# Kernel tuning notes

Measured on AMD Instinct MI355X. Metric: run time of the kernel, lower is better.

Reference implementation:

```python
import jax, jax.numpy as jnp
import numpy as np
from math import sqrt

DIM = 64
N_HEADS = 12
B, T = 4, 2048


def setup_inputs() -> dict:
    key = jax.random.key(0)
    ks = jax.random.split(key, 5)
    scale = 1.0 / sqrt(DIM)
    x = jax.random.normal(ks[0], (B, T, DIM), dtype=jnp.float32)
    # torch Linear(dim, h*dim) weight is (h*dim, dim); store transposed (dim, h*dim)
    Wq = jax.random.uniform(ks[1], (DIM, N_HEADS * DIM), dtype=jnp.float32, minval=-scale, maxval=scale)
    Wk = jax.random.uniform(ks[2], (DIM, N_HEADS * DIM), dtype=jnp.float32, minval=-scale, maxval=scale)
    Wv = jax.random.uniform(ks[3], (DIM, N_HEADS * DIM), dtype=jnp.float32, minval=-scale, maxval=scale)
    # finalDense: Linear(h*dim, dim) -> stored (h*dim, dim)
    Wo = jax.random.uniform(ks[4], (N_HEADS * DIM, DIM), dtype=jnp.float32,
                            minval=-1.0 / sqrt(N_HEADS * DIM), maxval=1.0 / sqrt(N_HEADS * DIM))
    return {"x": x, "Wq": Wq, "Wk": Wk, "Wv": Wv, "Wo": Wo}


def reference(x, Wq, Wk, Wv, Wo):
    b, t, k = x.shape
    h = Wq.shape[1] // k
    # NOTE: the original module does .view(b,t,h,k).view(b*h,t,k), a flat
    # row-major memory reinterpretation (NOT a head transpose). jnp.reshape
    # is the same flat reshape, so this is faithful.
    Q = (x @ Wq).reshape(b * h, t, k)
    K = (x @ Wk).reshape(b * h, t, k)
    V = (x @ Wv).reshape(b * h, t, k)
    # W[b,i,j] = sum_k K[b,i,k] * Q[b,j,k], scaled; softmax over j (last dim)
    W = jnp.einsum('bik,bjk->bij', K, Q) / sqrt(k)
    W = jax.nn.softmax(W, axis=2)
    Z = jnp.einsum('bij,bjk->bik', W, V)  # (b*h, t, k)
    Z = Z.reshape(b, t, h * k)  # flat reinterpretation, matches torch views
    return Z @ Wo
```

## Files before the change

### kernel.cpp

```cpp
#include <hip/hip_runtime.h>
#include <hip/hip_bf16.h>


#define DIM 64
#define NH 12
#define HD 768
#define BT 8192
#define TSEQ 2048
#define NSLICE 48
#define SLICE (TSEQ*DIM)

#define LDQ 72
#define LDP 72
#define LDT 72

typedef unsigned short ushort;
typedef __attribute__((ext_vector_type(8))) short bf16x8;
typedef __attribute__((ext_vector_type(4))) float f32x4;

#define SCALE2 0.18033688011112042f

__device__ __forceinline__ ushort f2b(float f) {
    union { float f; unsigned int i; } v; v.f = f;
    unsigned int x = v.i;
    return (ushort)((x + 0x7fffu + ((x >> 16) & 1u)) >> 16);
}

__global__ __launch_bounds__(256) void prep_w(
    const float* __restrict__ Wq, const float* __restrict__ Wk,
    const float* __restrict__ Wv, const float* __restrict__ Wo,
    ushort* __restrict__ Wt, ushort* __restrict__ Wot)
{
    __shared__ float tile[64][65];
    int bx = blockIdx.x;
    int z = bx / 12, bt = bx % 12;
    const float* __restrict__ IN = (z == 0) ? Wq : (z == 1) ? Wk : (z == 2) ? Wv : Wo;
    int inStride  = (z < 3) ? HD : DIM;
    int outStride = (z < 3) ? DIM : HD;
    int rbase = (z < 3) ? 0 : bt * 64;
    int cbase = (z < 3) ? bt * 64 : 0;
    ushort* __restrict__ OUT = (z < 3) ? (Wt + (size_t)z * HD * DIM) : Wot;
    int t = threadIdx.x;
    int r = t >> 2, c0 = (t & 3) * 16;
    #pragma unroll
    for (int cc = 0; cc < 16; cc += 4) {
        float4 a = *(const float4*)&IN[(size_t)(rbase + r) * inStride + cbase + c0 + cc];
        tile[r][c0 + cc] = a.x; tile[r][c0 + cc + 1] = a.y;
        tile[r][c0 + cc + 2] = a.z; tile[r][c0 + cc + 3] = a.w;
    }
    __syncthreads();
    int cl = t >> 2, r0 = (t & 3) * 16;
    ushort tmp[16] __attribute__((aligned(16)));
    #pragma unroll
    for (int rr = 0; rr < 16; ++rr) tmp[rr] = f2b(tile[r0 + rr][cl]);
    *(float4*)&OUT[(size_t)(cbase + cl) * outStride + rbase + r0] = *(const float4*)tmp;
    *(float4*)&OUT[(size_t)(cbase + cl) * outStride + rbase + r0 + 8] = *(const float4*)&tmp[8];
}

__global__ __launch_bounds__(256) void qkv_kernel(
    const float* __restrict__ x, const ushort* __restrict__ Wt,
    ushort* __restrict__ Q, ushort* __restrict__ K, ushort* __restrict__ V)
{
    int rt = blockIdx.x, yg = blockIdx.y;
    int t = threadIdx.x, w = t >> 6, lane = t & 63;
    int ln = lane & 15, q = lane >> 4;
    int m0 = rt * 64 + w * 16;

    float4 xa = *(const float4*)&x[(size_t)(m0 + ln) * DIM + q * 8];
    float4 xb_ = *(const float4*)&x[(size_t)(m0 + ln) * DIM + q * 8 + 4];
    float4 xc = *(const float4*)&x[(size_t)(m0 + ln) * DIM + 32 + q * 8];
    float4 xd = *(const float4*)&x[(size_t)(m0 + ln) * DIM + 32 + q * 8 + 4];
    ushort ta[8] __attribute__((aligned(16)));
    ushort tb[8] __attribute__((aligned(16)));
    ta[0]=f2b(xa.x); ta[1]=f2b(xa.y); ta[2]=f2b(xa.z); ta[3]=f2b(xa.w);
    ta[4]=f2b(xb_.x); ta[5]=f2b(xb_.y); ta[6]=f2b(xb_.z); ta[7]=f2b(xb_.w);
    tb[0]=f2b(xc.x); tb[1]=f2b(xc.y); tb[2]=f2b(xc.z); tb[3]=f2b(xc.w);
    tb[4]=f2b(xd.x); tb[5]=f2b(xd.y); tb[6]=f2b(xd.z); tb[7]=f2b(xd.w);
    bf16x8 af0 = *(const bf16x8*)ta;
    bf16x8 af1 = *(const bf16x8*)tb;

    for (int cc = 0; cc < 6; ++cc) {
        int ct = yg * 6 + cc;
        int which = ct / 12;
        int col0 = (ct % 12) * 64;
        const ushort* __restrict__ Wz = Wt + (size_t)which * HD * DIM;
        ushort* __restrict__ Y = (which == 0) ? Q : (which == 1) ? K : V;
        float sc = (which == 0) ? SCALE2 : 1.f;
        #pragma unroll
        for (int nt = 0; nt < 4; ++nt) {
            int n = col0 + nt * 16 + ln;
            bf16x8 bf0 = *(const bf16x8*)&Wz[(size_t)n * DIM + q * 8];
            bf16x8 bf1 = *(const bf16x8*)&Wz[(size_t)n * DIM + 32 + q * 8];
            f32x4 acc = (f32x4){0.f, 0.f, 0.f, 0.f};
            acc = __builtin_amdgcn_mfma_f32_16x16x32_bf16(af0, bf0, acc, 0, 0, 0);
            acc = __builtin_amdgcn_mfma_f32_16x16x32_bf16(af1, bf1, acc, 0, 0, 0);
            #pragma unroll
            for (int r = 0; r < 4; ++r)
                Y[(size_t)(m0 + q * 4 + r) * HD + col0 + nt * 16 + ln] = f2b(acc[r] * sc);
        }
    }
}

__global__ __launch_bounds__(256) void vtrans_kernel(
    const ushort* __restrict__ V, ushort* __restrict__ Vt)
{
    __shared__ ushort tileT[64 * LDT];
    int tt = blockIdx.x, s = blockIdx.y;
    const ushort* __restrict__ Vp = V + (size_t)s * SLICE;
    ushort* __restrict__ Vo = Vt + (size_t)s * SLICE;
    int t = threadIdx.x;
    int r = t >> 3, c = (t & 7) * 8;
    ushort va[8] __attribute__((aligned(16)));
    ushort vb[8] __attribute__((aligned(16)));
    *(float4*)va = *(const float4*)&Vp[(size_t)(tt * 64 + r) * DIM + c];
    *(float4*)vb = *(const float4*)&Vp[(size_t)(tt * 64 + r + 32) * DIM + c];
    int g0 = ((r >> 3) ^ (c >> 3)) * 8 + (r & 7);
    int g1 = (((r + 32) >> 3) ^ (c >> 3)) * 8 + (r & 7);
    #pragma unroll
    for (int k = 0; k < 8; ++k) {
        tileT[(c + k) * LDT + g0] = va[k];
        tileT[(c + k) * LDT + g1] = vb[k];
    }
    __syncthreads();
    #pragma unroll
    for (int j = 0; j < 2; ++j) {
        int flat = t + 256 * j;
        int d = flat >> 3, tg = flat & 7;
        int sg = tg ^ ((d >> 3) & 7);
        float4 vv = *(const float4*)&tileT[d * LDT + sg * 8];
        *(float4*)&Vo[(size_t)d * TSEQ + tt * 64 + tg * 8] = vv;
    }
}

__global__ __launch_bounds__(256) void attn_kernel(
    const ushort* __restrict__ Qs, const ushort* __restrict__ Ks,
    const ushort* __restrict__ Vts, ushort* __restrict__ Zs)
{
    __shared__ ushort Qt[64 * LDQ];
    __shared__ ushort Vtile[64 * LDQ];
    __shared__ ushort Pw[128 * LDP];
    int itile = blockIdx.x, s = blockIdx.y;
    const ushort* __restrict__ Qp = Qs + (size_t)s * SLICE;
    const ushort* __restrict__ Kp = Ks + (size_t)s * SLICE;
    const ushort* __restrict__ Vp = Vts + (size_t)s * SLICE;
    ushort* __restrict__ Zp = Zs + (size_t)s * SLICE;
    int t = threadIdx.x, w = t >> 6, lane = t & 63;
    int ln = lane & 15, q = lane >> 4;

    bf16x8 kf[2][2];
    #pragma unroll
    for (int ih = 0; ih < 2; ++ih) {
        int i0 = itile * 128 + w * 32 + ih * 16 + ln;
        kf[ih][0] = *(const bf16x8*)&Kp[(size_t)i0 * DIM + q * 8];
        kf[ih][1] = *(const bf16x8*)&Kp[(size_t)i0 * DIM + 32 + q * 8];
    }
    f32x4 Of[2][4];
    #pragma unroll
    for (int ih = 0; ih < 2; ++ih)
        #pragma unroll
        for (int dt = 0; dt < 4; ++dt) Of[ih][dt] = (f32x4){0.f, 0.f, 0.f, 0.f};
    float lsum[2] = {0.f, 0.f};
    ushort* Pme = &Pw[w * 32 * LDP];

    int sr = t >> 3, sc = (t & 7) * 8;
    float4 qa0 = *(const float4*)&Qp[(size_t)sr * DIM + sc];
    float4 qa1 = *(const float4*)&Qp[(size_t)(sr + 32) * DIM + sc];
    float4 va0 = *(const float4*)&Vp[(size_t)sr * TSEQ + sc];
    float4 va1 = *(const float4*)&Vp[(size_t)(sr + 32) * TSEQ + sc];

    for (int jt = 0; jt < TSEQ; jt += 64) {
        __syncthreads();
        *(float4*)&Qt[sr * LDQ + sc] = qa0;
        *(float4*)&Qt[(sr + 32) * LDQ + sc] = qa1;
        *(float4*)&Vtile[sr * LDQ + sc] = va0;
        *(float4*)&Vtile[(sr + 32) * LDQ + sc] = va1;
        __syncthreads();
        if (jt + 64 < TSEQ) {
            qa0 = *(const float4*)&Qp[(size_t)(jt + 64 + sr) * DIM + sc];
            qa1 = *(const float4*)&Qp[(size_t)(jt + 64 + sr + 32) * DIM + sc];
            va0 = *(const float4*)&Vp[(size_t)sr * TSEQ + jt + 64 + sc];
            va1 = *(const float4*)&Vp[(size_t)(sr + 32) * TSEQ + jt + 64 + sc];
        }

        f32x4 Sf[2][4];
        #pragma unroll
        for (int mt = 0; mt < 4; ++mt) {
            bf16x8 a0 = *(const bf16x8*)&Qt[(mt * 16 + ln) * LDQ + q * 8];
            bf16x8 a1 = *(const bf16x8*)&Qt[(mt * 16 + ln) * LDQ + 32 + q * 8];
            #pragma unroll
            for (int ih = 0; ih < 2; ++ih) {
                f32x4 acc = (f32x4){0.f, 0.f, 0.f, 0.f};
                acc = __builtin_amdgcn_mfma_f32_16x16x32_bf16(a0, kf[ih][0], acc, 0, 0, 0);
                acc = __builtin_amdgcn_mfma_f32_16x16x32_bf16(a1, kf[ih][1], acc, 0, 0, 0);
                Sf[ih][mt] = acc;
            }
        }
        #pragma unroll
        for (int ih = 0; ih < 2; ++ih) {
            float ls = 0.f;
            #pragma unroll
            for (int mt = 0; mt < 4; ++mt) {
                float p0 = __builtin_amdgcn_exp2f(Sf[ih][mt][0]);
                float p1 = __builtin_amdgcn_exp2f(Sf[ih][mt][1]);
                float p2 = __builtin_amdgcn_exp2f(Sf[ih][mt][2]);
                float p3 = __builtin_amdgcn_exp2f(Sf[ih][mt][3]);
                unsigned int b0 = __float_as_uint(p0), b1 = __float_as_uint(p1);
                unsigned int b2 = __float_as_uint(p2), b3 = __float_as_uint(p3);
                unsigned int t1 = b1 & 0xFFFF0000u, t3 = b3 & 0xFFFF0000u;
                unsigned int h01 = (b0 >> 16) | t1;
                unsigned int h23 = (b2 >> 16) | t3;
                ls += __uint_as_float(h01 << 16) + __uint_as_float(t1)
                    + __uint_as_float(h23 << 16) + __uint_as_float(t3);
                *(uint2*)&Pme[(ih * 16 + ln) * LDP + mt * 16 + q * 4] =
                    make_uint2(h01, h23);
            }
            lsum[ih] += ls;
        }
        bf16x8 pa[2][2];
        #pragma unroll
        for (int ih = 0; ih < 2; ++ih) {
            pa[ih][0] = *(const bf16x8*)&Pme[(ih * 16 + ln) * LDP + q * 8];
            pa[ih][1] = *(const bf16x8*)&Pme[(ih * 16 + ln) * LDP + 32 + q * 8];
        }
        #pragma unroll
        for (int dt = 0; dt < 4; ++dt) {
            bf16x8 vb0 = *(const bf16x8*)&Vtile[(dt * 16 + ln) * LDQ + q * 8];
            bf16x8 vb1 = *(const bf16x8*)&Vtile[(dt * 16 + ln) * LDQ + 32 + q * 8];
            #pragma unroll
            for (int ih = 0; ih < 2; ++ih) {
                Of[ih][dt] = __builtin_amdgcn_mfma_f32_16x16x32_bf16(pa[ih][0], vb0, Of[ih][dt], 0, 0, 0);
                Of[ih][dt] = __builtin_amdgcn_mfma_f32_16x16x32_bf16(pa[ih][1], vb1, Of[ih][dt], 0, 0, 0);
            }
        }
    }
    float linv_r[2][4];
    #pragma unroll
    for (int ih = 0; ih < 2; ++ih) {
        float l = lsum[ih];
        l += __shfl_xor(l, 16);
        l += __shfl_xor(l, 32);
        float linv = 1.f / l;
        #pragma unroll
        for (int r = 0; r < 4; ++r) linv_r[ih][r] = __shfl(linv, q * 4 + r);
    }
    #pragma unroll
    for (int ih = 0; ih < 2; ++ih)
        #pragma unroll
        for (int dt = 0; dt < 4; ++dt)
            #pragma unroll
            for (int r = 0; r < 4; ++r)
                Pme[(ih * 16 + q * 4 + r) * LDP + dt * 16 + ln] =
                    f2b(Of[ih][dt][r] * linv_r[ih][r]);
    __syncthreads();
    int zr = t >> 1, zc = (t & 1) * 32;
    size_t zoff = (size_t)(itile * 128 + zr) * DIM + zc;
    #pragma unroll
    for (int c4 = 0; c4 < 4; ++c4)
        *(float4*)&Zp[zoff + c4 * 8] = *(const float4*)&Pw[zr * LDP + zc + c4 * 8];
}

__global__ __launch_bounds__(64) void out_kernel(
    const ushort* __restrict__ Z, const ushort* __restrict__ Wot,
    float* __restrict__ out)
{
    int m0 = blockIdx.x * 32;
    int lane = threadIdx.x;
    int ln = lane & 15, q = lane >> 4;
    f32x4 acc[2][4];
    #pragma unroll
    for (int u = 0; u < 2; ++u)
        #pragma unroll
        for (int nt = 0; nt < 4; ++nt) acc[u][nt] = (f32x4){0.f, 0.f, 0.f, 0.f};
    for (int kc = 0; kc < 24; ++kc) {
        bf16x8 a0 = *(const bf16x8*)&Z[(size_t)(m0 + ln) * HD + kc * 32 + q * 8];
        bf16x8 a1 = *(const bf16x8*)&Z[(size_t)(m0 + 16 + ln) * HD + kc * 32 + q * 8];
        #pragma unroll
        for (int nt = 0; nt < 4; ++nt) {
            bf16x8 bf = *(const bf16x8*)&Wot[(size_t)(nt * 16 + ln) * HD + kc * 32 + q * 8];
            acc[0][nt] = __builtin_amdgcn_mfma_f32_16x16x32_bf16(a0, bf, acc[0][nt], 0, 0, 0);
            acc[1][nt] = __builtin_amdgcn_mfma_f32_16x16x32_bf16(a1, bf, acc[1][nt], 0, 0, 0);
        }
    }
    #pragma unroll
    for (int u = 0; u < 2; ++u)
        #pragma unroll
        for (int nt = 0; nt < 4; ++nt)
            #pragma unroll
            for (int r = 0; r < 4; ++r)
                out[(size_t)(m0 + u * 16 + q * 4 + r) * DIM + nt * 16 + ln] = acc[u][nt][r];
}

extern "C" void kernel_launch(void* const* d_in, const int* in_sizes, int n_in,
                              void* d_out, int out_size, void* d_ws, size_t ws_size,
                              hipStream_t stream)
{
    const float* x  = (const float*)d_in[0];
    const float* Wq = (const float*)d_in[1];
    const float* Wk = (const float*)d_in[2];
    const float* Wv = (const float*)d_in[3];
    const float* Wo = (const float*)d_in[4];
    float* out = (float*)d_out;

    const size_t n = (size_t)BT * HD;
    ushort* Q   = (ushort*)d_ws;
    ushort* K   = Q + n;
    ushort* V   = K + n;
    ushort* Vt  = V + n;
    ushort* Wt  = Vt;
    ushort* Wot = Vt + n;
    ushort* Z   = V;

    prep_w<<<48, 256, 0, stream>>>(Wq, Wk, Wv, Wo, Wt, Wot);
    qkv_kernel<<<dim3(128, 6), 256, 0, stream>>>(x, Wt, Q, K, V);
    vtrans_kernel<<<dim3(32, 48), 256, 0, stream>>>(V, Vt);
    attn_kernel<<<dim3(16, 48), 256, 0, stream>>>(Q, K, Vt, Z);
    out_kernel<<<256, 64, 0, stream>>>(Z, Wot, out);
}
```

Measured before the change: 181.5 us.

## Switch attention to 32x32x16 MFMA with register-resident P and double-buffered tiles

Rewrites the attention inner loop to use 32x32x16 bf16 MFMA instead of 16x16x32. The exponentiated scores are packed straight into register A-operands, so the LDS round-trip for P goes away. Q and V tiles are double-buffered in shared memory, which leaves one barrier per iteration instead of two. It also asks for 3 blocks per CU via launch bounds, which could force register spills, and the V operand reads become 4-element LDS loads that may bank-conflict.

Result: faster. 173.5 us (-4.4%).

```diff
diff --git a/kernel.cpp b/kernel.cpp
--- a/kernel.cpp
+++ b/kernel.cpp
@@ -11,12 +11,15 @@
 #define SLICE (TSEQ*DIM)
 
 #define LDQ 72
+#define LDT 72
 #define LDP 72
-#define LDT 72
 
 typedef unsigned short ushort;
 typedef __attribute__((ext_vector_type(8))) short bf16x8;
+typedef __attribute__((ext_vector_type(4))) short bf16x4;
 typedef __attribute__((ext_vector_type(4))) float f32x4;
+typedef __attribute__((ext_vector_type(16))) float f32x16;
+typedef __attribute__((ext_vector_type(4))) unsigned int uint32x4;
 
 #define SCALE2 0.18033688011112042f
 
@@ -132,131 +135,136 @@
     }
 }
 
-__global__ __launch_bounds__(256) void attn_kernel(
+__global__ __launch_bounds__(256, 3) void attn_kernel(
     const ushort* __restrict__ Qs, const ushort* __restrict__ Ks,
     const ushort* __restrict__ Vts, ushort* __restrict__ Zs)
 {
-    __shared__ ushort Qt[64 * LDQ];
-    __shared__ ushort Vtile[64 * LDQ];
-    __shared__ ushort Pw[128 * LDP];
+    __shared__ ushort sh[4 * 64 * LDQ];
     int itile = blockIdx.x, s = blockIdx.y;
     const ushort* __restrict__ Qp = Qs + (size_t)s * SLICE;
     const ushort* __restrict__ Kp = Ks + (size_t)s * SLICE;
     const ushort* __restrict__ Vp = Vts + (size_t)s * SLICE;
     ushort* __restrict__ Zp = Zs + (size_t)s * SLICE;
     int t = threadIdx.x, w = t >> 6, lane = t & 63;
-    int ln = lane & 15, q = lane >> 4;
-
-    bf16x8 kf[2][2];
-    #pragma unroll
-    for (int ih = 0; ih < 2; ++ih) {
-        int i0 = itile * 128 + w * 32 + ih * 16 + ln;
-        kf[ih][0] = *(const bf16x8*)&Kp[(size_t)i0 * DIM + q * 8];
-        kf[ih][1] = *(const bf16x8*)&Kp[(size_t)i0 * DIM + 32 + q * 8];
-    }
-    f32x4 Of[2][4];
-    #pragma unroll
-    for (int ih = 0; ih < 2; ++ih)
-        #pragma unroll
-        for (int dt = 0; dt < 4; ++dt) Of[ih][dt] = (f32x4){0.f, 0.f, 0.f, 0.f};
-    float lsum[2] = {0.f, 0.f};
-    ushort* Pme = &Pw[w * 32 * LDP];
+    int i5 = lane & 31, hi = lane >> 5;
+
+    bf16x8 kf[4];
+    {
+        size_t krow = (size_t)(itile * 128 + w * 32 + i5) * DIM;
+        #pragma unroll
+        for (int c = 0; c < 4; ++c)
+            kf[c] = *(const bf16x8*)&Kp[krow + c * 16 + hi * 8];
+    }
+
+    f32x16 Of0, Of1;
+    #pragma unroll
+    for (int r = 0; r < 16; ++r) { Of0[r] = 0.f; Of1[r] = 0.f; }
+    float lsum = 0.f;
 
     int sr = t >> 3, sc = (t & 7) * 8;
-    float4 qa0 = *(const float4*)&Qp[(size_t)sr * DIM + sc];
-    float4 qa1 = *(const float4*)&Qp[(size_t)(sr + 32) * DIM + sc];
-    float4 va0 = *(const float4*)&Vp[(size_t)sr * TSEQ + sc];
-    float4 va1 = *(const float4*)&Vp[(size_t)(sr + 32) * TSEQ + sc];
-
-    for (int jt = 0; jt < TSEQ; jt += 64) {
-        __syncthreads();
-        *(float4*)&Qt[sr * LDQ + sc] = qa0;
-        *(float4*)&Qt[(sr + 32) * LDQ + sc] = qa1;
-        *(float4*)&Vtile[sr * LDQ + sc] = va0;
-        *(float4*)&Vtile[(sr + 32) * LDQ + sc] = va1;
-        __syncthreads();
-        if (jt + 64 < TSEQ) {
-            qa0 = *(const float4*)&Qp[(size_t)(jt + 64 + sr) * DIM + sc];
-            qa1 = *(const float4*)&Qp[(size_t)(jt + 64 + sr + 32) * DIM + sc];
-            va0 = *(const float4*)&Vp[(size_t)sr * TSEQ + jt + 64 + sc];
-            va1 = *(const float4*)&Vp[(size_t)(sr + 32) * TSEQ + jt + 64 + sc];
-        }
-
-        f32x4 Sf[2][4];
-        #pragma unroll
-        for (int mt = 0; mt < 4; ++mt) {
-            bf16x8 a0 = *(const bf16x8*)&Qt[(mt * 16 + ln) * LDQ + q * 8];
-            bf16x8 a1 = *(const bf16x8*)&Qt[(mt * 16 + ln) * LDQ + 32 + q * 8];
-            #pragma unroll
-            for (int ih = 0; ih < 2; ++ih) {
-                f32x4 acc = (f32x4){0.f, 0.f, 0.f, 0.f};
-                acc = __builtin_amdgcn_mfma_f32_16x16x32_bf16(a0, kf[ih][0], acc, 0, 0, 0);
-                acc = __builtin_amdgcn_mfma_f32_16x16x32_bf16(a1, kf[ih][1], acc, 0, 0, 0);
-                Sf[ih][mt] = acc;
+    const ushort* qsrc0 = &Qp[(size_t)sr * DIM + sc];
+    const ushort* qsrc1 = &Qp[(size_t)(sr + 32) * DIM + sc];
+    const ushort* vsrc0 = &Vp[(size_t)sr * TSEQ + sc];
+    const ushort* vsrc1 = &Vp[(size_t)(sr + 32) * TSEQ + sc];
+
+    float4 qa0 = *(const float4*)qsrc0;
+    float4 qa1 = *(const float4*)qsrc1;
+    float4 va0 = *(const float4*)vsrc0;
+    float4 va1 = *(const float4*)vsrc1;
+    *(float4*)&sh[sr * LDQ + sc] = qa0;
+    *(float4*)&sh[(sr + 32) * LDQ + sc] = qa1;
+    *(float4*)&sh[2 * 64 * LDQ + sr * LDQ + sc] = va0;
+    *(float4*)&sh[2 * 64 * LDQ + (sr + 32) * LDQ + sc] = va1;
+    qa0 = *(const float4*)(qsrc0 + 64 * DIM);
+    qa1 = *(const float4*)(qsrc1 + 64 * DIM);
+    va0 = *(const float4*)(vsrc0 + 64);
+    va1 = *(const float4*)(vsrc1 + 64);
+    __syncthreads();
+
+    for (int tt = 0; tt < 32; ++tt) {
+        int ib = tt & 1;
+        const ushort* Qc = sh + ib * (64 * LDQ);
+        const ushort* Vc = sh + (2 + ib) * (64 * LDQ);
+        if (tt < 31) {
+            ushort* Qn = sh + (ib ^ 1) * (64 * LDQ);
+            ushort* Vn = sh + (2 + (ib ^ 1)) * (64 * LDQ);
+            *(float4*)&Qn[sr * LDQ + sc] = qa0;
+            *(float4*)&Qn[(sr + 32) * LDQ + sc] = qa1;
+            *(float4*)&Vn[sr * LDQ + sc] = va0;
+            *(float4*)&Vn[(sr + 32) * LDQ + sc] = va1;
+            if (tt < 30) {
+                size_t qo = (size_t)(tt + 2) * 64 * DIM;
+                int vo = (tt + 2) * 64;
+                qa0 = *(const float4*)(qsrc0 + qo);
+                qa1 = *(const float4*)(qsrc1 + qo);
+                va0 = *(const float4*)(vsrc0 + vo);
+                va1 = *(const float4*)(vsrc1 + vo);
             }
         }
         #pragma unroll
-        for (int ih = 0; ih < 2; ++ih) {
+        for (int js = 0; js < 2; ++js) {
+            f32x16 acc;
+            #pragma unroll
+            for (int r = 0; r < 16; ++r) acc[r] = 0.f;
+            #pragma unroll
+            for (int c = 0; c < 4; ++c) {
+                bf16x8 aQ = *(const bf16x8*)&Qc[(js * 32 + i5) * LDQ + c * 16 + hi * 8];
+                acc = __builtin_amdgcn_mfma_f32_32x32x16_bf16(aQ, kf[c], acc, 0, 0, 0);
+            }
+            unsigned wv[8];
             float ls = 0.f;
             #pragma unroll
-            for (int mt = 0; mt < 4; ++mt) {
-                float p0 = __builtin_amdgcn_exp2f(Sf[ih][mt][0]);
-                float p1 = __builtin_amdgcn_exp2f(Sf[ih][mt][1]);
-                float p2 = __builtin_amdgcn_exp2f(Sf[ih][mt][2]);
-                float p3 = __builtin_amdgcn_exp2f(Sf[ih][mt][3]);
+            for (int k = 0; k < 8; ++k) {
+                float p0 = __builtin_amdgcn_exp2f(acc[2 * k]);
+                float p1 = __builtin_amdgcn_exp2f(acc[2 * k + 1]);
                 unsigned int b0 = __float_as_uint(p0), b1 = __float_as_uint(p1);
-                unsigned int b2 = __float_as_uint(p2), b3 = __float_as_uint(p3);
-                unsigned int t1 = b1 & 0xFFFF0000u, t3 = b3 & 0xFFFF0000u;
-                unsigned int h01 = (b0 >> 16) | t1;
-                unsigned int h23 = (b2 >> 16) | t3;
-                ls += __uint_as_float(h01 << 16) + __uint_as_float(t1)
-                    + __uint_as_float(h23 << 16) + __uint_as_float(t3);
-                *(uint2*)&Pme[(ih * 16 + ln) * LDP + mt * 16 + q * 4] =
-                    make_uint2(h01, h23);
+                unsigned int t1 = b1 & 0xFFFF0000u;
+                unsigned int h = (b0 >> 16) | t1;
+                ls += __uint_as_float(h << 16) + __uint_as_float(t1);
+                wv[k] = h;
             }
-            lsum[ih] += ls;
-        }
-        bf16x8 pa[2][2];
-        #pragma unroll
-        for (int ih = 0; ih < 2; ++ih) {
-            pa[ih][0] = *(const bf16x8*)&Pme[(ih * 16 + ln) * LDP + q * 8];
-            pa[ih][1] = *(const bf16x8*)&Pme[(ih * 16 + ln) * LDP + 32 + q * 8];
-        }
-        #pragma unroll
-        for (int dt = 0; dt < 4; ++dt) {
-            bf16x8 vb0 = *(const bf16x8*)&Vtile[(dt * 16 + ln) * LDQ + q * 8];
-            bf16x8 vb1 = *(const bf16x8*)&Vtile[(dt * 16 + ln) * LDQ + 32 + q * 8];
-            #pragma unroll
-            for (int ih = 0; ih < 2; ++ih) {
-                Of[ih][dt] = __builtin_amdgcn_mfma_f32_16x16x32_bf16(pa[ih][0], vb0, Of[ih][dt], 0, 0, 0);
-                Of[ih][dt] = __builtin_amdgcn_mfma_f32_16x16x32_bf16(pa[ih][1], vb1, Of[ih][dt], 0, 0, 0);
+            lsum += ls;
+            uint32x4 u0 = { wv[0], wv[1], wv[2], wv[3] };
+            uint32x4 u1 = { wv[4], wv[5], wv[6], wv[7] };
+            bf16x8 pa0 = __builtin_bit_cast(bf16x8, u0);
+            bf16x8 pa1 = __builtin_bit_cast(bf16x8, u1);
+            #pragma unroll
+            for (int dt = 0; dt < 2; ++dt) {
+                int vbase = (dt * 32 + i5) * LDQ + js * 32 + 4 * hi;
+                bf16x4 v0a = *(const bf16x4*)&Vc[vbase];
+                bf16x4 v0b = *(const bf16x4*)&Vc[vbase + 8];
+                bf16x4 v1a = *(const bf16x4*)&Vc[vbase + 16];
+                bf16x4 v1b = *(const bf16x4*)&Vc[vbase + 24];
+                bf16x8 vb0 = __builtin_shufflevector(v0a, v0b, 0, 1, 2, 3, 4, 5, 6, 7);
+                bf16x8 vb1 = __builtin_shufflevector(v1a, v1b, 0, 1, 2, 3, 4, 5, 6, 7);
+                if (dt == 0) {
+                    Of0 = __builtin_amdgcn_mfma_f32_32x32x16_bf16(pa0, vb0, Of0, 0, 0, 0);
+                    Of0 = __builtin_amdgcn_mfma_f32_32x32x16_bf16(pa1, vb1, Of0, 0, 0, 0);
+                } else {
+                    Of1 = __builtin_amdgcn_mfma_f32_32x32x16_bf16(pa0, vb0, Of1, 0, 0, 0);
+                    Of1 = __builtin_amdgcn_mfma_f32_32x32x16_bf16(pa1, vb1, Of1, 0, 0, 0);
+                }
             }
         }
-    }
-    float linv_r[2][4];
-    #pragma unroll
-    for (int ih = 0; ih < 2; ++ih) {
-        float l = lsum[ih];
-        l += __shfl_xor(l, 16);
-        l += __shfl_xor(l, 32);
-        float linv = 1.f / l;
-        #pragma unroll
-        for (int r = 0; r < 4; ++r) linv_r[ih][r] = __shfl(linv, q * 4 + r);
-    }
-    #pragma unroll
-    for (int ih = 0; ih < 2; ++ih)
-        #pragma unroll
-        for (int dt = 0; dt < 4; ++dt)
-            #pragma unroll
-            for (int r = 0; r < 4; ++r)
-                Pme[(ih * 16 + q * 4 + r) * LDP + dt * 16 + ln] =
-                    f2b(Of[ih][dt][r] * linv_r[ih][r]);
+        __syncthreads();
+    }
+
+    float l = lsum + __shfl_xor(lsum, 32);
+    float linv = 1.f / l;
+    #pragma unroll
+    for (int r = 0; r < 16; ++r) {
+        int cr = (r & 3) + 8 * (r >> 2);
+        float li = __shfl(linv, cr + 4 * hi);
+        int row = w * 32 + cr + 4 * hi;
+        sh[row * LDQ + i5]      = f2b(Of0[r] * li);
+        sh[row * LDQ + 32 + i5] = f2b(Of1[r] * li);
+    }
     __syncthreads();
     int zr = t >> 1, zc = (t & 1) * 32;
     size_t zoff = (size_t)(itile * 128 + zr) * DIM + zc;
     #pragma unroll
     for (int c4 = 0; c4 < 4; ++c4)
-        *(float4*)&Zp[zoff + c4 * 8] = *(const float4*)&Pw[zr * LDP + zc + c4 * 8];
+        *(float4*)&Zp[zoff + c4 * 8] = *(const float4*)&sh[zr * LDQ + zc + c4 * 8];
 }
 
 __global__ __launch_bounds__(64) void out_kernel(
```
